# Kernel tuning notes

Measured on AMD Instinct MI355X. Metric: run time of the kernel, lower is better.

The kernel has to match this reference:

```python
import jax, jax.numpy as jnp
import numpy as np

N_EMBDS = 1024
N_HEADS = 16
HEAD_DIM = N_EMBDS // N_HEADS


def setup_inputs() -> dict:
    key = jax.random.key(0)
    ks = jax.random.split(key, 5)
    B, T, C = 2, 2048, N_EMBDS
    x = jax.random.normal(ks[0], (B, T, C), dtype=jnp.float32)
    s = 1.0 / np.sqrt(C)
    W_attn = jax.random.normal(ks[1], (C, 3 * C), dtype=jnp.float32) * s
    b_attn = jnp.zeros((3 * C,), dtype=jnp.float32)
    W_proj = jax.random.normal(ks[2], (C, C), dtype=jnp.float32) * s
    b_proj = jnp.zeros((C,), dtype=jnp.float32)
    return {"x": x, "W_attn": W_attn, "b_attn": b_attn, "W_proj": W_proj, "b_proj": b_proj}


def reference(x, W_attn, b_attn, W_proj, b_proj):
    B, T, C = x.shape
    H, D = N_HEADS, HEAD_DIM
    qkv = x @ W_attn + b_attn  # [B, T, 3C]
    q, k, v = jnp.split(qkv, 3, axis=-1)
    # [B, H, T, D]
    q = q.reshape(B, T, H, D).transpose(0, 2, 1, 3)
    k = k.reshape(B, T, H, D).transpose(0, 2, 1, 3)
    v = v.reshape(B, T, H, D).transpose(0, 2, 1, 3)
    att = jnp.einsum('bhqd,bhkd->bhqk', q, k) * (1.0 / np.sqrt(D))  # [B,H,T,T]
    causal = jnp.tril(jnp.ones((T, T), dtype=bool))
    att = jnp.where(causal[None, None], att, -jnp.inf)
    att = jax.nn.softmax(att, axis=-1)
    y = jnp.einsum('bhqk,bhkd->bhqd', att, v)  # [B,H,T,D]
    y = y.transpose(0, 2, 1, 3).reshape(B, T, C)
    return y @ W_proj + b_proj
```

## Files before the change

### kernel.cpp

```cpp
#include <hip/hip_runtime.h>
#include <hip/hip_bf16.h>


typedef __bf16 bf16x8 __attribute__((ext_vector_type(8)));
typedef float  f32x4  __attribute__((ext_vector_type(4)));
#define BF16 __hip_bfloat16

constexpr int Bb = 2, Tt = 2048, Cc = 1024, Hh = 16, Dd = 64;
constexpr float NEG_INF = -1e30f;
constexpr float Q_SCALE = 0.18033688011112042f;
constexpr float EXP2_BIAS = 17.312340490667562f;

__device__ __forceinline__ f32x4 mfma16(bf16x8 a, bf16x8 b, f32x4 c) {
  return __builtin_amdgcn_mfma_f32_16x16x32_bf16(a, b, c, 0, 0, 0);
}

__device__ __forceinline__ float fast_exp2(float x) {
  float r;
  asm("v_exp_f32 %0, %1" : "=v"(r) : "v"(x));
  return r;
}

__device__ __forceinline__ void gll16(const void* g, void* l) {
  __builtin_amdgcn_global_load_lds((const __attribute__((address_space(1))) void*)g,
                                   (__attribute__((address_space(3))) void*)l,
                                   16, 0, 0);
}

__device__ __forceinline__ int kperm_inv7(int r) {
  return (r & 0x63) | ((r & 0x0C) << 1) | ((r & 0x10) >> 2);
}

__global__ void prep_kernel(const float* __restrict__ x, BF16* __restrict__ xb,
                            const float* __restrict__ Wa, BF16* __restrict__ WaT,
                            const float* __restrict__ Wp, BF16* __restrict__ WpT) {
  __shared__ float tile[32][33];
  const int bx = blockIdx.x, tid = threadIdx.x;
  if (bx < 2048) {
    const int i = (bx * 256 + tid) * 8;
    const float4 a = *(const float4*)&x[i];
    const float4 b = *(const float4*)&x[i + 4];
    BF16 o[8];
    o[0] = __float2bfloat16(a.x); o[1] = __float2bfloat16(a.y);
    o[2] = __float2bfloat16(a.z); o[3] = __float2bfloat16(a.w);
    o[4] = __float2bfloat16(b.x); o[5] = __float2bfloat16(b.y);
    o[6] = __float2bfloat16(b.z); o[7] = __float2bfloat16(b.w);
    *(uint4*)&xb[i] = *(const uint4*)o;
    return;
  }
  const float* in; BF16* outT; int K, N, gx, gy;
  if (bx < 5120) {
    const int idx = bx - 2048;
    in = Wa; outT = WaT; K = 1024; N = 3072; gx = idx % 96; gy = idx / 96;
  } else {
    const int idx = bx - 5120;
    in = Wp; outT = WpT; K = 1024; N = 1024; gx = idx % 32; gy = idx / 32;
  }
  const int n0 = gx * 32, k0 = gy * 32;
  const int tx = tid & 31, ty = tid >> 5;
#pragma unroll
  for (int i = ty; i < 32; i += 8) tile[i][tx] = in[(size_t)(k0 + i) * N + (n0 + tx)];
  __syncthreads();
#pragma unroll
  for (int i = ty; i < 32; i += 8)
    outT[(size_t)(n0 + i) * K + (k0 + tx)] = __float2bfloat16(tile[tx][i]);
}

template <int MODE>
__global__ __launch_bounds__(256) void gemm_bt(const BF16* __restrict__ A,
                                               const BF16* __restrict__ Bt,
                                               const float* __restrict__ bias,
                                               BF16* __restrict__ oq,
                                               BF16* __restrict__ ok,
                                               BF16* __restrict__ ov,
                                               float* __restrict__ fout,
                                               int Ndim, int Kdim) {
  __shared__ alignas(16) BF16 sA[128 * 64];
  __shared__ alignas(16) BF16 sB[128 * 64];
  const int tid = threadIdx.x;
  const int wave = tid >> 6, lane = tid & 63;
  const int quad = lane >> 4, l16 = lane & 15;
  const int wm = (wave >> 1) * 64, wn = (wave & 1) * 64;
  const int bm = blockIdx.y * 128, bn = blockIdx.x * 128;
  const int sw = l16 & 7;

  f32x4 acc[4][4];
#pragma unroll
  for (int i = 0; i < 4; ++i)
#pragma unroll
    for (int j = 0; j < 4; ++j) acc[i][j] = f32x4{0.f, 0.f, 0.f, 0.f};

  const int srow = wave * 32 + (lane >> 3);
  const int sgl = (lane ^ (lane >> 3)) & 7;
  const BF16* gA0 = &A[(size_t)(bm + srow) * Kdim + sgl * 8];
  const BF16* gB0 = &Bt[(size_t)(bn + srow) * Kdim + sgl * 8];
  const size_t rstep8 = (size_t)8 * Kdim;

  for (int k0 = 0; k0 < Kdim; k0 += 64) {
    __syncthreads();
#pragma unroll
    for (int s = 0; s < 4; ++s) {
      gll16(gA0 + s * rstep8 + k0, &sA[wave * 2048 + s * 512]);
      gll16(gB0 + s * rstep8 + k0, &sB[wave * 2048 + s * 512]);
    }
    __syncthreads();

#pragma unroll
    for (int h = 0; h < 2; ++h) {
      bf16x8 af[4], bf_[4];
#pragma unroll
      for (int i = 0; i < 4; ++i)
        af[i] = *(const bf16x8*)
            &sA[(wm + i * 16 + l16) * 64 + (((h * 4 + quad) ^ sw) << 3)];
#pragma unroll
      for (int j = 0; j < 4; ++j)
        bf_[j] = *(const bf16x8*)
            &sB[(wn + j * 16 + l16) * 64 + (((h * 4 + quad) ^ sw) << 3)];
#pragma unroll
      for (int i = 0; i < 4; ++i)
#pragma unroll
        for (int j = 0; j < 4; ++j) acc[i][j] = mfma16(af[i], bf_[j], acc[i][j]);
    }
  }

#pragma unroll
  for (int j = 0; j < 4; ++j) {
    const int gn = bn + wn + j * 16 + l16;
    const float bsv = bias[gn];
    if (MODE == 1) {
#pragma unroll
      for (int i = 0; i < 4; ++i)
#pragma unroll
        for (int r = 0; r < 4; ++r) {
          const int gm = bm + wm + i * 16 + quad * 4 + r;
          fout[(size_t)gm * Ndim + gn] = acc[i][j][r] + bsv;
        }
    } else {
      const int which = (bn + wn + j * 16) >> 10;
      const int c = gn & 1023;
      const int hh = c >> 6, dd = c & 63;
#pragma unroll
      for (int i = 0; i < 4; ++i) {
        const int gm0 = bm + wm + i * 16 + quad * 4;
        const int bb = gm0 >> 11, tk0 = gm0 & 2047;
        const size_t bh = (size_t)(bb * Hh + hh);
        if (which == 2) {
          BF16 tmp[4];
#pragma unroll
          for (int r = 0; r < 4; ++r) tmp[r] = __float2bfloat16(acc[i][j][r] + bsv);
          *(uint2*)&ov[(bh * Dd + dd) * Tt + tk0] = *(const uint2*)tmp;
        } else {
          BF16* dst = (which == 0) ? oq : ok;
          const float scale = (which == 0) ? Q_SCALE : 1.0f;
#pragma unroll
          for (int r = 0; r < 4; ++r)
            dst[(bh * Tt + tk0 + r) * Dd + dd] =
                __float2bfloat16((acc[i][j][r] + bsv) * scale);
        }
      }
    }
  }
}

__global__ __launch_bounds__(256) void attn_kernel(const BF16* __restrict__ qg,
                                                   const BF16* __restrict__ kg,
                                                   const BF16* __restrict__ vtg,
                                                   BF16* __restrict__ yb) {
  __shared__ alignas(16) BF16 sK[2 * 8192];
  __shared__ alignas(16) BF16 sV[2 * 8192];
  const int id = blockIdx.x;
  const int xcd = id & 7, local = id >> 3;
  const int bh = xcd * 4 + (local & 3);
  const int s = 31 - (local >> 2);
  const int b = bh >> 4, h = bh & 15;
  const int tid = threadIdx.x;
  const int wave = tid >> 6, lane = tid & 63;
  const int quad = lane >> 4, l16 = lane & 15;
  const size_t base = ((size_t)(b * Hh + h)) * Tt * Dd;
  const int qrow0 = s * 64 + wave * 16;
  const int sw = l16 & 7;

  bf16x8 qf0, qf1;
  {
    const size_t off = base + (size_t)(qrow0 + l16) * Dd;
    qf0 = *(const bf16x8*)&qg[off + quad * 8];
    qf1 = *(const bf16x8*)&qg[off + 32 + quad * 8];
  }

  bf16x8 ones8;
#pragma unroll
  for (int j = 0; j < 8; ++j) ones8[j] = (__bf16)1.0f;

  f32x4 o[4], oL;
#pragma unroll
  for (int i = 0; i < 4; ++i) o[i] = f32x4{0.f, 0.f, 0.f, 0.f};
  oL = f32x4{0.f, 0.f, 0.f, 0.f};

  const f32x4 cbias = f32x4{-EXP2_BIAS, -EXP2_BIAS, -EXP2_BIAS, -EXP2_BIAS};

  const int t = tid;
  const int sgk = (t ^ (t >> 3)) & 7;
  const int sgv = (t ^ (t >> 4)) & 15;
  const BF16* pk[4];
  const BF16* pv[4];
#pragma unroll
  for (int i = 0; i < 4; ++i) {
    pk[i] = &kg[base + (size_t)kperm_inv7(i * 32 + (t >> 3)) * Dd + sgk * 8];
    pv[i] = &vtg[base + (size_t)(i * 16 + (t >> 4)) * Tt + sgv * 8];
  }

#define STAGE_K(buf, tt_)                                            \
  do {                                                               \
    const size_t ko_ = (size_t)(tt_) * 8192;                         \
    _Pragma("unroll") for (int i_ = 0; i_ < 4; ++i_)                 \
        gll16(pk[i_] + ko_, &sK[(buf) * 8192 + i_ * 2048 + t * 8]);  \
  } while (0)
#define STAGE_V(buf, tt_)                                            \
  do {                                                               \
    const int vo_ = (tt_) * 128;                                     \
    _Pragma("unroll") for (int i_ = 0; i_ < 4; ++i_)                 \
        gll16(pv[i_] + vo_, &sV[(buf) * 8192 + i_ * 2048 + t * 8]);  \
  } while (0)

#define QK_TILE(jt_)                                                        \
  do {                                                                      \
    const BF16* sKb_ = &sK[((jt_) & 1) * 8192];                             \
    __builtin_amdgcn_s_setprio(1);                                          \
    _Pragma("unroll") for (int tt = 0; tt < 8; ++tt) {                      \
      const bf16x8 kf0 =                                                    \
          *(const bf16x8*)&sKb_[(tt * 16 + l16) * 64 + ((quad ^ sw) << 3)]; \
      const bf16x8 kf1 = *(const bf16x8*)                                   \
          &sKb_[(tt * 16 + l16) * 64 + (((4 + quad) ^ sw) << 3)];           \
      sS[tt] = mfma16(kf0, qf0, cbias);                                     \
      sS[tt] = mfma16(kf1, qf1, sS[tt]);                                    \
    }                                                                       \
    __builtin_amdgcn_s_setprio(0);                                          \
  } while (0)

#define MASK_TILE(jt_)                                                  \
  do {                                                                  \
    const int kb_ = (jt_) * 128;                                        \
    const int q_ = qrow0 + l16;                                         \
    _Pragma("unroll") for (int tt = 0; tt < 8; ++tt) {                  \
      const int kc0 = kb_ + (tt >> 1) * 32 + quad * 8 + (tt & 1) * 4;   \
      _Pragma("unroll") for (int r = 0; r < 4; ++r)                     \
          if (kc0 + r > q_) sS[tt][r] = NEG_INF;                        \
    }                                                                   \
  } while (0)

#define EXP_P()                                                         \
  do {                                                                  \
    _Pragma("unroll") for (int cc = 0; cc < 4; ++cc)                    \
        _Pragma("unroll") for (int j = 0; j < 8; ++j)                   \
            pf[cc][j] = (__bf16)fast_exp2(sS[cc * 2 + (j >> 2)][j & 3]); \
  } while (0)

#define PV_TILE(jt_)                                                          \
  do {                                                                        \
    const BF16* sVb_ = &sV[((jt_) & 1) * 8192];                               \
    __builtin_amdgcn_s_setprio(1);                                            \
    _Pragma("unroll") for (int cc = 0; cc < 4; ++cc) {                        \
      _Pragma("unroll") for (int dt = 0; dt < 4; ++dt) {                      \
        const bf16x8 vb = *(const bf16x8*)                                    \
            &sVb_[(dt * 16 + l16) * 128 +                                     \
                  ((((cc * 4 + quad) ^ l16) & 15) << 3)];                     \
        o[dt] = mfma16(pf[cc], vb, o[dt]);                                    \
      }                                                                       \
      oL = mfma16(pf[cc], ones8, oL);                                         \
    }                                                                         \
    __builtin_amdgcn_s_setprio(0);                                            \
  } while (0)

  const int nt = (s + 2) >> 1;
  f32x4 sS[8];
  bf16x8 pf[4];

  STAGE_K(0, 0);

  asm volatile("s_waitcnt vmcnt(0)" ::: "memory");
  __builtin_amdgcn_s_barrier();
  STAGE_V(0, 0);
  if (nt > 1) STAGE_K(1, 1);
  QK_TILE(0);
  if (nt == 1) MASK_TILE(0);

  for (int jt = 1; jt < nt; ++jt) {
    asm volatile("s_waitcnt vmcnt(0)" ::: "memory");
    __builtin_amdgcn_s_barrier();
    STAGE_V(jt & 1, jt);
    if (jt + 1 < nt) STAGE_K((jt + 1) & 1, jt + 1);
    EXP_P();
    QK_TILE(jt);
    if (jt == nt - 1) MASK_TILE(jt);
    PV_TILE(jt - 1);
  }

  asm volatile("s_waitcnt vmcnt(0)" ::: "memory");
  __builtin_amdgcn_s_barrier();
  EXP_P();
  PV_TILE(nt - 1);

#undef STAGE_K
#undef STAGE_V
#undef QK_TILE
#undef MASK_TILE
#undef EXP_P
#undef PV_TILE

#pragma unroll
  for (int r = 0; r < 4; ++r) {
    const float inv = 1.0f / oL[r];
    const int trow = qrow0 + quad * 4 + r;
#pragma unroll
    for (int dt = 0; dt < 4; ++dt)
      yb[((size_t)(b * Tt + trow)) * Cc + h * Dd + dt * 16 + l16] =
          __float2bfloat16(o[dt][r] * inv);
  }
}

extern "C" void kernel_launch(void* const* d_in, const int* in_sizes, int n_in,
                              void* d_out, int out_size, void* d_ws, size_t ws_size,
                              hipStream_t stream) {
  (void)in_sizes; (void)n_in; (void)out_size; (void)ws_size;
  const float* x      = (const float*)d_in[0];
  const float* W_attn = (const float*)d_in[1];
  const float* b_attn = (const float*)d_in[2];
  const float* W_proj = (const float*)d_in[3];
  const float* b_proj = (const float*)d_in[4];
  float* out = (float*)d_out;

  constexpr size_t SZ_WA = (size_t)3072 * 1024;
  constexpr size_t SZ_WP = (size_t)1024 * 1024;
  constexpr size_t SZ_X  = (size_t)4096 * 1024;
  constexpr size_t SZ_T  = (size_t)Bb * Hh * Tt * Dd;

  BF16* ws   = (BF16*)d_ws;
  BF16* wtAb = ws;
  BF16* wtPb = wtAb + SZ_WA;
  BF16* xb   = wtPb + SZ_WP;
  BF16* q    = xb + SZ_X;
  BF16* k    = q + SZ_T;
  BF16* vt   = k + SZ_T;
  BF16* yb   = vt + SZ_T;

  prep_kernel<<<dim3(6144), 256, 0, stream>>>(x, xb, W_attn, wtAb, W_proj, wtPb);
  gemm_bt<0><<<dim3(24, 32), 256, 0, stream>>>(xb, wtAb, b_attn, q, k, vt, nullptr,
                                               3072, 1024);
  attn_kernel<<<dim3(1024), 256, 0, stream>>>(q, k, vt, yb);
  gemm_bt<1><<<dim3(8, 32), 256, 0, stream>>>(yb, wtPb, b_proj, nullptr, nullptr,
                                              nullptr, out, 1024, 1024);
}
```

Before: 167.4 us.

## Double-buffer GEMM shared-memory tiles to overlap global loads with MFMA

The projection GEMM kernel now uses two LDS buffers for the A and B tiles and prefetches the next K-tile through global_load_lds while MFMAs run on the current one. The two barriers per K step become one, using an explicit vmcnt wait plus s_barrier. It also raises wave priority around the MFMA block. This doubles LDS per block to 64KB, which may reduce occupancy. The single barrier must still keep the buffer being overwritten from being read by slower waves.

After: 172.8 us. 3.2% more time.

```diff
diff --git a/kernel.cpp b/kernel.cpp
--- a/kernel.cpp
+++ b/kernel.cpp
@@ -75,8 +75,8 @@
                                                BF16* __restrict__ ov,
                                                float* __restrict__ fout,
                                                int Ndim, int Kdim) {
-  __shared__ alignas(16) BF16 sA[128 * 64];
-  __shared__ alignas(16) BF16 sB[128 * 64];
+  __shared__ alignas(16) BF16 sA[2][128 * 64];
+  __shared__ alignas(16) BF16 sB[2][128 * 64];
   const int tid = threadIdx.x;
   const int wave = tid >> 6, lane = tid & 63;
   const int quad = lane >> 4, l16 = lane & 15;
@@ -96,14 +96,23 @@
   const BF16* gB0 = &Bt[(size_t)(bn + srow) * Kdim + sgl * 8];
   const size_t rstep8 = (size_t)8 * Kdim;
 
-  for (int k0 = 0; k0 < Kdim; k0 += 64) {
-    __syncthreads();
-#pragma unroll
-    for (int s = 0; s < 4; ++s) {
-      gll16(gA0 + s * rstep8 + k0, &sA[wave * 2048 + s * 512]);
-      gll16(gB0 + s * rstep8 + k0, &sB[wave * 2048 + s * 512]);
-    }
-    __syncthreads();
+#define GSTAGE(buf, k0_)                                                   \
+  do {                                                                     \
+    _Pragma("unroll") for (int s_ = 0; s_ < 4; ++s_) {                     \
+      gll16(gA0 + s_ * rstep8 + (k0_), &sA[buf][wave * 2048 + s_ * 512]);  \
+      gll16(gB0 + s_ * rstep8 + (k0_), &sB[buf][wave * 2048 + s_ * 512]);  \
+    }                                                                      \
+  } while (0)
+
+  const int KT = Kdim >> 6;
+  GSTAGE(0, 0);
+
+  for (int kt = 0; kt < KT; ++kt) {
+    asm volatile("s_waitcnt vmcnt(0)" ::: "memory");
+    __builtin_amdgcn_s_barrier();
+    const BF16* lA = sA[kt & 1];
+    const BF16* lB = sB[kt & 1];
+    if (kt + 1 < KT) GSTAGE((kt + 1) & 1, (kt + 1) * 64);
 
 #pragma unroll
     for (int h = 0; h < 2; ++h) {
@@ -111,17 +120,20 @@
 #pragma unroll
       for (int i = 0; i < 4; ++i)
         af[i] = *(const bf16x8*)
-            &sA[(wm + i * 16 + l16) * 64 + (((h * 4 + quad) ^ sw) << 3)];
+            &lA[(wm + i * 16 + l16) * 64 + (((h * 4 + quad) ^ sw) << 3)];
 #pragma unroll
       for (int j = 0; j < 4; ++j)
         bf_[j] = *(const bf16x8*)
-            &sB[(wn + j * 16 + l16) * 64 + (((h * 4 + quad) ^ sw) << 3)];
+            &lB[(wn + j * 16 + l16) * 64 + (((h * 4 + quad) ^ sw) << 3)];
+      __builtin_amdgcn_s_setprio(1);
 #pragma unroll
       for (int i = 0; i < 4; ++i)
 #pragma unroll
         for (int j = 0; j < 4; ++j) acc[i][j] = mfma16(af[i], bf_[j], acc[i][j]);
+      __builtin_amdgcn_s_setprio(0);
     }
   }
+#undef GSTAGE
 
 #pragma unroll
   for (int j = 0; j < 4; ++j) {
@@ -248,10 +260,10 @@
     }                                                                   \
   } while (0)
 
-#define EXP_P()                                                         \
-  do {                                                                  \
-    _Pragma("unroll") for (int cc = 0; cc < 4; ++cc)                    \
-        _Pragma("unroll") for (int j = 0; j < 8; ++j)                   \
+#define EXP_P()                                                          \
+  do {                                                                   \
+    _Pragma("unroll") for (int cc = 0; cc < 4; ++cc)                     \
+        _Pragma("unroll") for (int j = 0; j < 8; ++j)                    \
             pf[cc][j] = (__bf16)fast_exp2(sS[cc * 2 + (j >> 2)][j & 3]); \
   } while (0)
 
```
